# Optimization experiments

Hardware: AMD Instinct MI355X
Metric: run time of the kernel (lower is better)

The kernel has to match this reference:

```python
import jax, jax.numpy as jnp
import numpy as np

N, E, G = 50000, 1600000, 64
F_NODE, F_EDGE, ACT = 128, 16, 10
NEG_SLOPE = 0.2  # GATv2Conv default negative_slope
LAYER_DIMS = [(F_NODE, 32), (32, 64), (64, 128)]


def _glorot(k, shape):
    fan_in, fan_out = shape[0], shape[-1]
    s = jnp.sqrt(6.0 / (fan_in + fan_out))
    return jax.random.uniform(k, shape, jnp.float32, -s, s)


def setup_inputs() -> dict:
    key = jax.random.key(0)
    ks = iter(jax.random.split(key, 64))
    inp = {
        "x": jax.random.normal(next(ks), (N, F_NODE), jnp.float32),
        "edge_attr": jax.random.normal(next(ks), (E, F_EDGE), jnp.float32),
        "edge_index": jax.random.randint(next(ks), (2, E), 0, N, jnp.int32),
        "batch": jnp.sort(jax.random.randint(next(ks), (N,), 0, G, jnp.int32)),
    }
    for i, (din, dout) in enumerate(LAYER_DIMS, 1):
        inp[f"Wl{i}"] = _glorot(next(ks), (din, dout))   # lin_l (source transform)
        inp[f"bl{i}"] = jnp.zeros((dout,), jnp.float32)
        inp[f"Wr{i}"] = _glorot(next(ks), (din, dout))   # lin_r (dest transform)
        inp[f"br{i}"] = jnp.zeros((dout,), jnp.float32)
        inp[f"We{i}"] = _glorot(next(ks), (F_EDGE, dout))  # lin_edge (no bias)
        inp[f"att{i}"] = _glorot(next(ks), (1, dout))[0]   # attention vector
        inp[f"bo{i}"] = jnp.zeros((dout,), jnp.float32)    # output bias
    inp["Wv1"] = _glorot(next(ks), (128, 64)); inp["bv1"] = jnp.zeros((64,), jnp.float32)
    inp["Wv2"] = _glorot(next(ks), (64, 1));   inp["bv2"] = jnp.zeros((1,), jnp.float32)
    inp["Wa1"] = _glorot(next(ks), (128, 64)); inp["ba1"] = jnp.zeros((64,), jnp.float32)
    inp["Wa2"] = _glorot(next(ks), (64, ACT)); inp["ba2"] = jnp.zeros((ACT,), jnp.float32)
    return inp


def _gatv2(x, src, dst, ea, Wl, bl, Wr, br, We, att, bo):
    """GATv2Conv, heads=1, concat=True, edge_dim=F_EDGE (eval mode)."""
    xl = x @ Wl + bl                               # [N, D] source-side
    xr = x @ Wr + br                               # [N, D] dest-side
    m = xl[src] + xr[dst] + ea @ We                # [E, D]
    score = (jax.nn.leaky_relu(m, NEG_SLOPE) * att).sum(-1)  # [E]
    # segment softmax over edges grouped by destination node
    mx = jax.lax.stop_gradient(jax.ops.segment_max(score, dst, num_segments=N))
    ex = jnp.exp(score - mx[dst])
    den = jax.ops.segment_sum(ex, dst, num_segments=N)
    alpha = ex / (den[dst] + 1e-16)                # [E]
    out = jax.ops.segment_sum(alpha[:, None] * xl[src], dst, num_segments=N)
    return out + bo


def _forward(x, edge_attr, src, dst, batch, p):
    h = x
    for i in (1, 2, 3):
        h = jax.nn.relu(_gatv2(h, src, dst, edge_attr,
                               p[f"Wl{i}"], p[f"bl{i}"], p[f"Wr{i}"], p[f"br{i}"],
                               p[f"We{i}"], p[f"att{i}"], p[f"bo{i}"]))
    # global mean pool per graph
    cnt = jax.ops.segment_sum(jnp.ones((N,), h.dtype), batch, num_segments=G)
    pooled = jax.ops.segment_sum(h, batch, num_segments=G) / jnp.maximum(cnt, 1.0)[:, None]
    # dueling heads
    v = jax.nn.relu(pooled @ p["Wv1"] + p["bv1"]) @ p["Wv2"] + p["bv2"]      # [G, 1]
    a = jax.nn.relu(pooled @ p["Wa1"] + p["ba1"]) @ p["Wa2"] + p["ba2"]      # [G, ACT]
    return v + (a - a.mean(axis=1, keepdims=True))


def reference(x, edge_attr, edge_index, batch,
              Wl1, bl1, Wr1, br1, We1, att1, bo1,
              Wl2, bl2, Wr2, br2, We2, att2, bo2,
              Wl3, bl3, Wr3, br3, We3, att3, bo3,
              Wv1, bv1, Wv2, bv2, Wa1, ba1, Wa2, ba2):
    p = dict(Wl1=Wl1, bl1=bl1, Wr1=Wr1, br1=br1, We1=We1, att1=att1, bo1=bo1,
             Wl2=Wl2, bl2=bl2, Wr2=Wr2, br2=br2, We2=We2, att2=att2, bo2=bo2,
             Wl3=Wl3, bl3=bl3, Wr3=Wr3, br3=br3, We3=We3, att3=att3, bo3=bo3,
             Wv1=Wv1, bv1=bv1, Wv2=Wv2, bv2=bv2, Wa1=Wa1, ba1=ba1, Wa2=Wa2, ba2=ba2)
    return _forward(x, edge_attr, edge_index[0], edge_index[1], batch, p)
```

## Files before the change

kernel.cpp:

```cpp
#include <hip/hip_runtime.h>
#include <cstdint>
#include <cstddef>

static constexpr int NN = 50000;
static constexpr int NE = 1600000;
static constexpr int NG = 64;
static constexpr int FE = 16;
static constexpr float SLOPE = 0.2f;

template<int DIN, int DOUT>
__global__ __launch_bounds__(256) void k_node_linear(
    const float* __restrict__ h,
    const float* __restrict__ Wl, const float* __restrict__ bl,
    const float* __restrict__ Wr, const float* __restrict__ br,
    float* __restrict__ xl, float* __restrict__ xr)
{
    __shared__ float sW[2 * DIN * DOUT];
    __shared__ float sX[16 * DIN];
    const int n0 = blockIdx.x * 16;

    for (int i = threadIdx.x; i < DIN * DOUT; i += 256) {
        sW[i] = Wl[i];
        sW[DIN * DOUT + i] = Wr[i];
    }
    for (int i = threadIdx.x; i < 16 * DIN; i += 256) {
        int r = i / DIN, k = i % DIN;
        int n = n0 + r;
        sX[i] = (n < NN) ? h[(size_t)n * DIN + k] : 0.0f;
    }
    __syncthreads();

    for (int o = threadIdx.x; o < 16 * DOUT; o += 256) {
        int r = o / DOUT, d = o % DOUT;
        int n = n0 + r;
        if (n >= NN) continue;
        float accl = bl[d], accr = br[d];
        #pragma unroll 8
        for (int k = 0; k < DIN; ++k) {
            float xv = sX[r * DIN + k];
            accl = fmaf(xv, sW[k * DOUT + d], accl);
            accr = fmaf(xv, sW[DIN * DOUT + k * DOUT + d], accr);
        }
        xl[(size_t)n * DOUT + d] = accl;
        xr[(size_t)n * DOUT + d] = accr;
    }
}

__global__ __launch_bounds__(256) void k_count(
    const int* __restrict__ ei, int* __restrict__ cnt)
{
    const int e = blockIdx.x * 256 + threadIdx.x;
    if (e >= NE) return;
    atomicAdd(cnt + ei[NE + e], 1);
}

__global__ __launch_bounds__(1024) void k_scan(
    const int* __restrict__ cnt, int* __restrict__ rowptr)
{
    __shared__ int part[1024];
    const int T = 1024;
    const int C = (NN + T - 1) / T;
    const int t = threadIdx.x;
    const int base = t * C;
    int s = 0;
    for (int i = 0; i < C; ++i) {
        int idx = base + i;
        if (idx < NN) s += cnt[idx];
    }
    part[t] = s;
    __syncthreads();
    for (int off = 1; off < T; off <<= 1) {
        int v = 0;
        if (t >= off) v = part[t - off];
        __syncthreads();
        if (t >= off) part[t] += v;
        __syncthreads();
    }
    int run = (t == 0) ? 0 : part[t - 1];
    for (int i = 0; i < C; ++i) {
        int idx = base + i;
        if (idx < NN) { rowptr[idx] = run; run += cnt[idx]; }
    }
    if (t == T - 1) rowptr[NN] = run;
}

__global__ __launch_bounds__(256) void k_fill(
    const int* __restrict__ ei, const int* __restrict__ rowptr,
    int* __restrict__ woff, int* __restrict__ eids, int* __restrict__ esrc)
{
    const int e = blockIdx.x * 256 + threadIdx.x;
    if (e >= NE) return;
    const int dst = ei[NE + e];
    const int pos = rowptr[dst] + atomicAdd(woff + dst, 1);
    eids[pos] = e;
    esrc[pos] = ei[e];
}

__global__ __launch_bounds__(256) void k_gather_ea(
    const int* __restrict__ eids, const float* __restrict__ ea,
    float* __restrict__ eap)
{
    const long long i = (long long)blockIdx.x * 256 + threadIdx.x;
    if (i >= (long long)NE * 4) return;
    const int p = (int)(i >> 2), q = (int)(i & 3);
    const int e = eids[p];
    *(float4*)(eap + (size_t)p * FE + q * 4) =
        *(const float4*)(ea + (size_t)e * FE + q * 4);
}

template<int D, bool PERM>
__global__ __launch_bounds__(128, 4) void k_gat_fused(
    const int* __restrict__ rowptr, const int* __restrict__ eidx,
    const int* __restrict__ esrc, const float* __restrict__ eaf,
    const float* __restrict__ xl, const float* __restrict__ xr,
    const float* __restrict__ We, const float* __restrict__ att,
    const float* __restrict__ bo, float* __restrict__ hout)
{
    constexpr int SW  = D / 2;
    constexpr int EPW = 64 / SW;
    constexpr int WPB = 2;

    const int wave = threadIdx.x >> 6;
    const int lane = threadIdx.x & 63;
    const int n = blockIdx.x * WPB + wave;
    if (n >= NN) return;
    const int sub = lane / SW;
    const int dl  = lane % SW;
    const int d0  = 2 * dl;

    float rWe[2 * FE], rAtt[2], rXr[2], acc[2];
    {
        const float2 a2 = *(const float2*)(att + d0);
        rAtt[0] = a2.x; rAtt[1] = a2.y;
        const float2 x2 = *(const float2*)(xr + (size_t)n * D + d0);
        rXr[0] = x2.x; rXr[1] = x2.y;
        #pragma unroll
        for (int k = 0; k < FE; ++k) {
            const float2 w2 = *(const float2*)(We + k * D + d0);
            rWe[2 * k] = w2.x; rWe[2 * k + 1] = w2.y;
        }
        acc[0] = acc[1] = 0.f;
    }

    const int p0 = rowptr[n], p1 = rowptr[n + 1];
    float m = -3.4e38f, l = 0.f;

    auto load_edge = [&](int p, float (&eav)[FE], float (&rXl)[2]) {
        const int s = esrc[p];
        const float2 x2 = *(const float2*)(xl + (size_t)s * D + d0);
        rXl[0] = x2.x; rXl[1] = x2.y;
        int erow; if constexpr (PERM) erow = p; else erow = eidx[p];
        if constexpr (SW == 64) {
            const float* ep = eaf + (size_t)(unsigned)__builtin_amdgcn_readfirstlane(erow) * FE;
            #pragma unroll
            for (int k = 0; k < FE; ++k) eav[k] = ep[k];
        } else {
            const float* ep = eaf + (size_t)erow * FE;
            #pragma unroll
            for (int k4 = 0; k4 < 4; ++k4) {
                const float4 v = *(const float4*)(ep + 4 * k4);
                eav[4 * k4]     = v.x; eav[4 * k4 + 1] = v.y;
                eav[4 * k4 + 2] = v.z; eav[4 * k4 + 3] = v.w;
            }
        }
    };
    auto score_edge = [&](const float (&eav)[FE], const float (&rXl)[2]) -> float {
        float m0 = rXl[0] + rXr[0], m1 = rXl[1] + rXr[1];
        #pragma unroll
        for (int k = 0; k < FE; ++k) {
            m0 = fmaf(eav[k], rWe[2 * k], m0);
            m1 = fmaf(eav[k], rWe[2 * k + 1], m1);
        }
        m0 = m0 > 0.f ? m0 : SLOPE * m0;
        m1 = m1 > 0.f ? m1 : SLOPE * m1;
        float sv = fmaf(m0, rAtt[0], m1 * rAtt[1]);
        #pragma unroll
        for (int off = 1; off < SW; off <<= 1) sv += __shfl_xor(sv, off);
        return sv;
    };
    auto sm_update = [&](float sv, const float (&rXl)[2]) {
        const float dd = sv - m;
        float wexp;
        if (__builtin_expect(dd > 8.f, 0)) {
            const float r = __expf(-dd);
            acc[0] *= r; acc[1] *= r;
            l *= r; m = sv; wexp = 1.f;
        } else {
            wexp = __expf(dd);
        }
        acc[0] = fmaf(wexp, rXl[0], acc[0]);
        acc[1] = fmaf(wexp, rXl[1], acc[1]);
        l += wexp;
    };

    int p = p0 + sub;
    for (; p + EPW < p1; p += 2 * EPW) {
        float eavA[FE], rXlA[2], eavB[FE], rXlB[2];
        load_edge(p, eavA, rXlA);
        load_edge(p + EPW, eavB, rXlB);
        const float svA = score_edge(eavA, rXlA);
        const float svB = score_edge(eavB, rXlB);
        sm_update(svA, rXlA);
        sm_update(svB, rXlB);
    }
    if (p < p1) {
        float eav[FE], rXl[2];
        load_edge(p, eav, rXl);
        sm_update(score_edge(eav, rXl), rXl);
    }

    #pragma unroll
    for (int step = SW; step < 64; step <<= 1) {
        const float mo = __shfl_xor(m, step);
        const float mstar = fmaxf(m, mo);
        const float sc = __expf(m - mstar);
        acc[0] *= sc; acc[1] *= sc; l *= sc;
        acc[0] += __shfl_xor(acc[0], step);
        acc[1] += __shfl_xor(acc[1], step);
        l += __shfl_xor(l, step);
        m = mstar;
    }

    if (lane < SW) {
        const float inv = 1.0f / (l + 1e-16f);
        const float2 b2 = *(const float2*)(bo + d0);
        float2 o;
        o.x = fmaxf(fmaf(acc[0], inv, b2.x), 0.f);
        o.y = fmaxf(fmaf(acc[1], inv, b2.y), 0.f);
        *(float2*)(hout + (size_t)n * D + d0) = o;
    }
}

__global__ __launch_bounds__(128) void k_pool(
    const float* __restrict__ h, const int* __restrict__ batch,
    float* __restrict__ pooled, float* __restrict__ cnt)
{
    constexpr int BLOCKS = 512;
    constexpr int CH = (NN + BLOCKS - 1) / BLOCKS;
    const int t = threadIdx.x;
    const int n0 = blockIdx.x * CH;
    const int n1 = min(NN, n0 + CH);
    if (n0 >= n1) return;

    int g = batch[n0];
    float acc = 0.f, c = 0.f;
    for (int n = n0; n < n1; ++n) {
        const int bg = batch[n];
        if (bg != g) {
            atomicAdd(pooled + g * 128 + t, acc);
            if (t == 0) atomicAdd(cnt + g, c);
            acc = 0.f; c = 0.f; g = bg;
        }
        acc += h[(size_t)n * 128 + t];
        c += 1.f;
    }
    atomicAdd(pooled + g * 128 + t, acc);
    if (t == 0) atomicAdd(cnt + g, c);
}

__global__ __launch_bounds__(128) void k_head(
    const float* __restrict__ pooled, const float* __restrict__ cnt,
    const float* __restrict__ Wv1, const float* __restrict__ bv1,
    const float* __restrict__ Wv2, const float* __restrict__ bv2,
    const float* __restrict__ Wa1, const float* __restrict__ ba1,
    const float* __restrict__ Wa2, const float* __restrict__ ba2,
    float* __restrict__ out)
{
    __shared__ float pr[128];
    __shared__ float hv[64];
    __shared__ float ha[64];
    __shared__ float sA[10];
    __shared__ float sVM[2];
    const int g = blockIdx.x;
    const int t = threadIdx.x;

    const float inv = 1.0f / fmaxf(cnt[g], 1.0f);
    pr[t] = pooled[g * 128 + t] * inv;
    __syncthreads();

    if (t < 64) {
        float sv = bv1[t], sa = ba1[t];
        #pragma unroll 8
        for (int k = 0; k < 128; ++k) {
            float p = pr[k];
            sv = fmaf(p, Wv1[k * 64 + t], sv);
            sa = fmaf(p, Wa1[k * 64 + t], sa);
        }
        hv[t] = fmaxf(sv, 0.0f);
        ha[t] = fmaxf(sa, 0.0f);
    }
    __syncthreads();

    if (t < 10) {
        float av = ba2[t];
        #pragma unroll
        for (int j = 0; j < 64; ++j) av = fmaf(ha[j], Wa2[j * 10 + t], av);
        sA[t] = av;
    }
    if (t == 64) {
        float v = bv2[0];
        #pragma unroll
        for (int j = 0; j < 64; ++j) v = fmaf(hv[j], Wv2[j], v);
        sVM[0] = v;
    }
    __syncthreads();

    if (t == 0) {
        float s = 0.0f;
        #pragma unroll
        for (int j = 0; j < 10; ++j) s += sA[j];
        sVM[1] = s * 0.1f;
    }
    __syncthreads();

    if (t < 10) out[g * 10 + t] = sVM[0] + sA[t] - sVM[1];
}

extern "C" void kernel_launch(void* const* d_in, const int* in_sizes, int n_in,
                              void* d_out, int out_size, void* d_ws, size_t ws_size,
                              hipStream_t stream)
{
    const float* x     = (const float*)d_in[0];
    const float* ea    = (const float*)d_in[1];
    const int*   ei    = (const int*)d_in[2];
    const int*   batch = (const int*)d_in[3];

    float* ws = (float*)d_ws;
    float* xl     = ws;
    float* xr     = xl + (size_t)NN * 128;
    float* hA     = xr + (size_t)NN * 128;
    float* hB     = hA + (size_t)NN * 128;
    float* pooled = hB + (size_t)NN * 64;
    float* cntp   = pooled + (size_t)NG * 128;
    int*   rowptr = (int*)(cntp + NG);
    int*   cnt    = rowptr + (NN + 1);
    int*   woff   = cnt + NN;
    int*   eids   = woff + NN;
    int*   esrc   = eids + NE;
    float* eaperm = (float*)(esrc + NE);

    const size_t need = ((char*)(eaperm + (size_t)NE * FE)) - (char*)d_ws;
    const bool use_perm = (ws_size >= need);

    const int EB = (NE + 255) / 256;

    hipMemsetAsync(cnt, 0, NN * sizeof(int), stream);
    hipMemsetAsync(woff, 0, NN * sizeof(int), stream);
    k_count<<<dim3(EB), dim3(256), 0, stream>>>(ei, cnt);
    k_scan<<<dim3(1), dim3(1024), 0, stream>>>(cnt, rowptr);
    k_fill<<<dim3(EB), dim3(256), 0, stream>>>(ei, rowptr, woff, eids, esrc);
    if (use_perm) {
        const long long tot = (long long)NE * 4;
        k_gather_ea<<<dim3((unsigned)((tot + 255) / 256)), dim3(256), 0, stream>>>(
            eids, ea, eaperm);
    }

    const int GB = (NN + 1) / 2;

#define LAYER(DIN, DOUT, HIN, HOUT, B)                                                   \
    do {                                                                                 \
        k_node_linear<DIN, DOUT><<<dim3((NN + 15) / 16), dim3(256), 0, stream>>>(        \
            HIN, (const float*)d_in[B], (const float*)d_in[(B) + 1],                     \
            (const float*)d_in[(B) + 2], (const float*)d_in[(B) + 3], xl, xr);           \
        if (use_perm)                                                                    \
            k_gat_fused<DOUT, true><<<dim3(GB), dim3(128), 0, stream>>>(                 \
                rowptr, eids, esrc, eaperm, xl, xr, (const float*)d_in[(B) + 4],         \
                (const float*)d_in[(B) + 5], (const float*)d_in[(B) + 6], HOUT);         \
        else                                                                             \
            k_gat_fused<DOUT, false><<<dim3(GB), dim3(128), 0, stream>>>(                \
                rowptr, eids, esrc, ea, xl, xr, (const float*)d_in[(B) + 4],             \
                (const float*)d_in[(B) + 5], (const float*)d_in[(B) + 6], HOUT);         \
    } while (0)

    LAYER(128, 32, x,  hA, 4);
    LAYER(32,  64, hA, hB, 11);
    LAYER(64, 128, hB, hA, 18);

#undef LAYER

    hipMemsetAsync(pooled, 0, NG * 128 * sizeof(float), stream);
    hipMemsetAsync(cntp, 0, NG * sizeof(float), stream);
    k_pool<<<dim3(512), dim3(128), 0, stream>>>(hA, batch, pooled, cntp);
    k_head<<<dim3(NG), dim3(128), 0, stream>>>(
        pooled, cntp,
        (const float*)d_in[25], (const float*)d_in[26],
        (const float*)d_in[27], (const float*)d_in[28],
        (const float*)d_in[29], (const float*)d_in[30],
        (const float*)d_in[31], (const float*)d_in[32],
        (float*)d_out);
}
```

Measured before the change: 1.000 ms.

## Fuse edge-attribute permutation into CSR fill and merge adjacent memsets

The CSR fill kernel now copies each edge's 16-float attribute row straight to its destination-sorted slot, which removes the separate gather kernel and the eids write and read in the permuted path. Adjacent memsets for cnt/woff and pooled/cntp are merged into single calls, and the leaky-relu select becomes an fmaxf. The fused copy reads coalesced but writes scattered 64-byte rows, where the old gather did the opposite, so memory efficiency may move either way.

```diff
diff --git a/kernel.cpp b/kernel.cpp
--- a/kernel.cpp
+++ b/kernel.cpp
@@ -6,7 +6,8 @@
 static constexpr int NE = 1600000;
 static constexpr int NG = 64;
 static constexpr int FE = 16;
-static constexpr float SLOPE = 0.2f;
+
+typedef float f32x4 __attribute__((ext_vector_type(4)));
 
 template<int DIN, int DOUT>
 __global__ __launch_bounds__(256) void k_node_linear(
@@ -86,26 +87,21 @@
 
 __global__ __launch_bounds__(256) void k_fill(
     const int* __restrict__ ei, const int* __restrict__ rowptr,
-    int* __restrict__ woff, int* __restrict__ eids, int* __restrict__ esrc)
+    int* __restrict__ woff, int* __restrict__ eids, int* __restrict__ esrc,
+    const float* __restrict__ ea, float* __restrict__ eaperm, const int do_perm)
 {
     const int e = blockIdx.x * 256 + threadIdx.x;
     if (e >= NE) return;
     const int dst = ei[NE + e];
     const int pos = rowptr[dst] + atomicAdd(woff + dst, 1);
-    eids[pos] = e;
     esrc[pos] = ei[e];
-}
-
-__global__ __launch_bounds__(256) void k_gather_ea(
-    const int* __restrict__ eids, const float* __restrict__ ea,
-    float* __restrict__ eap)
-{
-    const long long i = (long long)blockIdx.x * 256 + threadIdx.x;
-    if (i >= (long long)NE * 4) return;
-    const int p = (int)(i >> 2), q = (int)(i & 3);
-    const int e = eids[p];
-    *(float4*)(eap + (size_t)p * FE + q * 4) =
-        *(const float4*)(ea + (size_t)e * FE + q * 4);
+    if (do_perm) {
+        const f32x4* s4 = (const f32x4*)(ea + (size_t)e * FE);
+        f32x4* d4 = (f32x4*)(eaperm + (size_t)pos * FE);
+        d4[0] = s4[0]; d4[1] = s4[1]; d4[2] = s4[2]; d4[3] = s4[3];
+    } else {
+        eids[pos] = e;
+    }
 }
 
 template<int D, bool PERM>
@@ -171,8 +167,8 @@
             m0 = fmaf(eav[k], rWe[2 * k], m0);
             m1 = fmaf(eav[k], rWe[2 * k + 1], m1);
         }
-        m0 = m0 > 0.f ? m0 : SLOPE * m0;
-        m1 = m1 > 0.f ? m1 : SLOPE * m1;
+        m0 = fmaxf(m0, 0.2f * m0);
+        m1 = fmaxf(m1, 0.2f * m1);
         float sv = fmaf(m0, rAtt[0], m1 * rAtt[1]);
         #pragma unroll
         for (int off = 1; off < SW; off <<= 1) sv += __shfl_xor(sv, off);
@@ -344,16 +340,11 @@
 
     const int EB = (NE + 255) / 256;
 
-    hipMemsetAsync(cnt, 0, NN * sizeof(int), stream);
-    hipMemsetAsync(woff, 0, NN * sizeof(int), stream);
+    hipMemsetAsync(cnt, 0, 2 * NN * sizeof(int), stream);
     k_count<<<dim3(EB), dim3(256), 0, stream>>>(ei, cnt);
     k_scan<<<dim3(1), dim3(1024), 0, stream>>>(cnt, rowptr);
-    k_fill<<<dim3(EB), dim3(256), 0, stream>>>(ei, rowptr, woff, eids, esrc);
-    if (use_perm) {
-        const long long tot = (long long)NE * 4;
-        k_gather_ea<<<dim3((unsigned)((tot + 255) / 256)), dim3(256), 0, stream>>>(
-            eids, ea, eaperm);
-    }
+    k_fill<<<dim3(EB), dim3(256), 0, stream>>>(
+        ei, rowptr, woff, eids, esrc, ea, eaperm, use_perm ? 1 : 0);
 
     const int GB = (NN + 1) / 2;
 
@@ -378,8 +369,7 @@
 
 #undef LAYER
 
-    hipMemsetAsync(pooled, 0, NG * 128 * sizeof(float), stream);
-    hipMemsetAsync(cntp, 0, NG * sizeof(float), stream);
+    hipMemsetAsync(pooled, 0, (NG * 128 + NG) * sizeof(float), stream);
     k_pool<<<dim3(512), dim3(128), 0, stream>>>(hA, batch, pooled, cntp);
     k_head<<<dim3(NG), dim3(128), 0, stream>>>(
         pooled, cntp,
```

Measured after the change: 1.003 ms. About the same (+0.2%).
